# Performance work log

Hardware: AMD Instinct MI355X
Metric: run time of the kernel (lower is better)

The kernel has to match this reference:

```python
import jax, jax.numpy as jnp
import numpy as np

B = 16384      # batch of Monte Carlo paths
N = 100        # time steps
DIM_W = 3
DT = 0.01
SQRT_DT = DT ** 0.5
SIGMA0 = 0.5   # constant diffusion coefficient (concrete sigma = SIGMA0 * ones(B,1,DIM_W))


def _mlp(x, W1, b1, W2, b2, W3, b3):
    h = jax.nn.relu(x @ W1 + b1)
    h = jax.nn.relu(h @ W2 + b2)
    return h @ W3 + b3


def setup_inputs() -> dict:
    key = jax.random.key(0)
    ks = jax.random.split(key, 8)
    s = 0.1  # modest weight scale for numerical sanity
    return {
        'y0': jnp.ones((1,), jnp.float32),
        'Y0': jnp.zeros((1, 1), jnp.float32),
        'zW1': s * jax.random.normal(ks[0], (2, 64), jnp.float32),
        'zb1': jnp.zeros((64,), jnp.float32),
        'zW2': s * jax.random.normal(ks[1], (64, 64), jnp.float32),
        'zb2': jnp.zeros((64,), jnp.float32),
        'zW3': s * jax.random.normal(ks[2], (64, 3), jnp.float32),
        'zb3': jnp.zeros((3,), jnp.float32),
        'qW1': s * jax.random.normal(ks[3], (2, 64), jnp.float32),
        'qb1': jnp.zeros((64,), jnp.float32),
        'qW2': s * jax.random.normal(ks[4], (64, 64), jnp.float32),
        'qb2': jnp.zeros((64,), jnp.float32),
        'qW3': s * jax.random.normal(ks[5], (64, 1), jnp.float32),
        'qb3': jnp.zeros((1,), jnp.float32),
        'dW': jax.random.normal(ks[6], (N, B, DIM_W), jnp.float32),
        'dZ': jax.random.normal(ks[7], (N, B, DIM_W), jnp.float32),
    }


def reference(y0, Y0, zW1, zb1, zW2, zb2, zW3, zb3,
              qW1, qb1, qW2, qb2, qW3, qb3, dW, dZ):
    y = jnp.broadcast_to(y0.reshape(1, 1), (B, 1))          # (B,1) state
    Y = jnp.broadcast_to(Y0, (B, 1))                         # (B,1) value process
    t = jnp.zeros((B, 1), jnp.float32)

    def step(carry, noise):
        y, Y, t, loss_acc = carry
        dWi, dZi = noise
        inp = jnp.concatenate([t, y], axis=1)                # (B,2)
        z = _mlp(inp, zW1, zb1, zW2, zb2, zW3, zb3)          # (B,3)
        q = _mlp(inp, qW1, qb1, qW2, qb2, qW3, qb3)          # (B,1)
        f = 0.5 * q * q                                      # generator (B,1)
        dw = dWi * SQRT_DT
        dz = dZi * SQRT_DT
        # sigma = SIGMA0 * ones(B,1,DIM_W); bmm(sigma, dw) = SIGMA0 * sum_j dw_j
        diffusion = SIGMA0 * jnp.sum(dw, axis=1, keepdims=True)
        y_new = y + q * DT + diffusion                       # mu = q
        Y_next = Y - f * DT + jnp.sum(z * dw, axis=1, keepdims=True)
        residual = Y_next - (Y - f * DT + jnp.sum(z * dz, axis=1, keepdims=True))
        loss_acc = loss_acc + jnp.mean(residual * residual)
        return (y_new, Y_next, t + DT, loss_acc), None

    (y, Y, t, total_residual_loss), _ = jax.lax.scan(
        step, (y, Y, t, jnp.float32(0.0)), (dW, dZ))
    terminal = y * y                                         # terminal_cost(y)
    terminal_loss = jnp.mean((Y - terminal) ** 2)
    return terminal_loss + total_residual_loss
```

## Files before the change

### kernel.cpp

```cpp
#include <hip/hip_runtime.h>
#include <hip/hip_bf16.h>

#define BATCH   16384
#define NSTEPS  100
#define DT_     0.01f
#define SQRTDT  0.1f
#define SIGMA0_ 0.5f

typedef _Float16  f16x2  __attribute__((ext_vector_type(2)));
typedef _Float16  f16x4  __attribute__((ext_vector_type(4)));
typedef _Float16  f16x8  __attribute__((ext_vector_type(8)));
typedef __fp16    h16x2  __attribute__((ext_vector_type(2)));
typedef float     f32x4  __attribute__((ext_vector_type(4)));

__global__ void zero_out_kernel(float* out) { if (threadIdx.x == 0) out[0] = 0.0f; }

static __device__ __forceinline__ f16x4 pk4(const f32x4& d) {
    union { h16x2 h[2]; f16x4 v; } c;
    c.h[0] = __builtin_amdgcn_cvt_pkrtz(d[0], d[1]);
    c.h[1] = __builtin_amdgcn_cvt_pkrtz(d[2], d[3]);
    return c.v;
}

struct N3 { float a, b, c; };

__launch_bounds__(256, 2)
__global__ void deepbsde_kernel(
    const float* __restrict__ y0,  const float* __restrict__ Y0,
    const float* __restrict__ zW1, const float* __restrict__ zb1,
    const float* __restrict__ zW2, const float* __restrict__ zb2,
    const float* __restrict__ zW3, const float* __restrict__ zb3,
    const float* __restrict__ qW1, const float* __restrict__ qb1,
    const float* __restrict__ qW2, const float* __restrict__ qb2,
    const float* __restrict__ qW3, const float* __restrict__ qb3,
    const float* __restrict__ dW,  const float* __restrict__ dZ,
    float* __restrict__ out)
{
    __shared__ __align__(16) _Float16 tbl[NSTEPS * 128];
    __shared__ float yring[2][NSTEPS + 1][16];
    __shared__ float ffin[2][16];
    __shared__ int   flags[2][2];

    const int tid  = threadIdx.x;
    const int lane = tid & 63;
    const int w    = tid >> 6;
    const int g    = w >> 1;
    const int flip = (((int)blockIdx.x >> 3) ^ ((int)blockIdx.x >> 8)) & 1;
    const bool isQ = ((w & 1) ^ flip) != 0;
    const int ln15 = lane & 15, q4 = lane >> 4;
    const int gw   = (blockIdx.x << 1) + g;
    const int pbase = gw << 4;

    if (tid < 4) ((int*)flags)[tid] = 0;

    {
        float tt = 0.0f;
        for (int i = 0; i < NSTEPS; ++i) {
            int r = (tid - (i << 6)) & 255;
            if (r < 64) {
                int q4e = r >> 4, mlp_ = (r >> 3) & 1, m = r & 7;
                const float* Wp = mlp_ ? qW1 : zW1;
                const float* bp = mlp_ ? qb1 : zb1;
                int i0 = 2*m, i1 = 2*m + 1;
                int k0 = 32*(i0 >> 3) + 8*q4e + (i0 & 7);
                int k1 = 32*(i1 >> 3) + 8*q4e + (i1 & 7);
                _Float16 th = (_Float16)tt;
                f16x2 A = {(_Float16)Wp[k0], (_Float16)Wp[k1]};
                f16x2 C = {(_Float16)bp[k0], (_Float16)bp[k1]};
                f16x2 tv = {th, th};
                f16x2 v = A*tv + C;
                int idx = (i*4 + q4e)*16 + mlp_*8 + m;
                *(f16x2*)&tbl[idx << 1] = v;
            }
            tt += DT_;
        }
    }

    const float* W1p = isQ ? qW1 : zW1;
    const float* W2p = isQ ? qW2 : zW2;
    const float* b2p = isQ ? qb2 : zb2;

    f16x2 B1[8];
#pragma unroll
    for (int m = 0; m < 8; ++m) {
        int i0 = 2*m, i1 = 2*m + 1;
        int k0 = 32*(i0 >> 3) + 8*q4 + (i0 & 7);
        int k1 = 32*(i1 >> 3) + 8*q4 + (i1 & 7);
        B1[m] = (f16x2){(_Float16)W1p[64 + k0], (_Float16)W1p[64 + k1]};
    }

    f16x8 Af[4][2];
#pragma unroll
    for (int tN = 0; tN < 4; ++tN)
#pragma unroll
        for (int f = 0; f < 2; ++f)
#pragma unroll
            for (int j = 0; j < 8; ++j) {
                int k = 32*f + 8*q4 + j, n = 16*tN + ln15;
                Af[tN][f][j] = (_Float16)W2p[k*64 + n];
            }

    f32x4 b2v[4];
#pragma unroll
    for (int tN = 0; tN < 4; ++tN)
#pragma unroll
        for (int r = 0; r < 4; ++r)
            b2v[tN][r] = b2p[16*tN + 4*q4 + r];

    const int c3 = ln15 & 3;
    f16x8 A3[2];
#pragma unroll
    for (int fl = 0; fl < 2; ++fl)
#pragma unroll
        for (int j = 0; j < 8; ++j) {
            int tN = 2*fl + (j >> 2);
            int n  = 16*tN + 4*q4 + (j & 3);
            float wv = isQ ? ((c3 == 3) ? qW3[n]                 : 0.0f)
                           : ((c3 < 3)  ? SQRTDT * zW3[n*3 + c3] : 0.0f);
            A3[fl][j] = (_Float16)wv;
        }

    const f32x4 C3b = isQ ? (f32x4){0.0f, 0.0f, 0.0f, qb3[0]}
                          : (f32x4){SQRTDT*zb3[0], SQRTDT*zb3[1], SQRTDT*zb3[2], 0.0f};

    const float CSIG = SIGMA0_ * SQRTDT;
    const float NHDT = -0.5f * DT_;
    const float y0v = y0[0], Y0v = Y0[0];

    const f16x2 zero2h = {(_Float16)0.0f, (_Float16)0.0f};
    const f16x4 zero4h = {(_Float16)0.0f, (_Float16)0.0f, (_Float16)0.0f, (_Float16)0.0f};

    if (isQ && q4 == 0) *(volatile float*)&yring[g][0][ln15] = y0v;

    __syncthreads();

    auto loadW = [&](int i, N3& d) {
        int ic = (i < NSTEPS) ? i : NSTEPS - 1;
        const float* p = dW + ((size_t)ic * BATCH + pbase + ln15) * 3;
        d.a = p[0]; d.b = p[1]; d.c = p[2];
    };
    auto loadZ = [&](int i, N3& d) {
        int ic = (i < NSTEPS) ? i : NSTEPS - 1;
        const float* p = dZ + ((size_t)ic * BATCH + pbase + ln15) * 3;
        d.a = p[0]; d.b = p[1]; d.c = p[2];
    };

    if (!isQ) {
        float Ysum = 0.0f, acc = 0.0f;
        float ya, yb, yc, yd;

        auto ybatch = [&](int base) {
            volatile int* qf = &flags[g][0];
            while (*qf < base + 4) { }
            ya = *(volatile float*)&yring[g][base + 0][ln15];
            yb = *(volatile float*)&yring[g][base + 1][ln15];
            yc = *(volatile float*)&yring[g][base + 2][ln15];
            yd = *(volatile float*)&yring[g][base + 3][ln15];
        };

        auto zpair = [&](int iA, float yA, int iB, float yB,
                         const N3& wA, const N3& zA, const N3& wB, const N3& zB) {
            const f16x8* tpA = (const f16x8*)(tbl + (iA*4 + q4)*32);
            const f16x8* tpB = (const f16x8*)(tbl + (iB*4 + q4)*32);
            union U8 { f16x8 v; f16x2 h[4]; };
            U8 TA0; TA0.v = tpA[0]; U8 TA1; TA1.v = tpA[1];
            U8 TB0; TB0.v = tpB[0]; U8 TB1; TB1.v = tpB[1];

            _Float16 yhA = (_Float16)yA, yhB = (_Float16)yB;
            const f16x2 yvA = {yhA, yhA}, yvB = {yhB, yhB};
            union { f16x2 h[4]; f16x8 v; } a0, a1, b0, b1;
#pragma unroll
            for (int m = 0; m < 4; ++m) {
                a0.h[m] = __builtin_elementwise_max((f16x2)(B1[m]*yvA   + TA0.h[m]), zero2h);
                b0.h[m] = __builtin_elementwise_max((f16x2)(B1[m]*yvB   + TB0.h[m]), zero2h);
                a1.h[m] = __builtin_elementwise_max((f16x2)(B1[m+4]*yvA + TA1.h[m]), zero2h);
                b1.h[m] = __builtin_elementwise_max((f16x2)(B1[m+4]*yvB + TB1.h[m]), zero2h);
            }

            union { f16x4 q[4]; f16x8 o[2]; } BA, BB;
#pragma unroll
            for (int tN = 0; tN < 4; ++tN) {
                f32x4 dA = b2v[tN];
                f32x4 dB = b2v[tN];
                dA = __builtin_amdgcn_mfma_f32_16x16x32_f16(Af[tN][0], a0.v, dA, 0, 0, 0);
                dB = __builtin_amdgcn_mfma_f32_16x16x32_f16(Af[tN][0], b0.v, dB, 0, 0, 0);
                dA = __builtin_amdgcn_mfma_f32_16x16x32_f16(Af[tN][1], a1.v, dA, 0, 0, 0);
                dB = __builtin_amdgcn_mfma_f32_16x16x32_f16(Af[tN][1], b1.v, dB, 0, 0, 0);
                BA.q[tN] = __builtin_elementwise_max(pk4(dA), zero4h);
                BB.q[tN] = __builtin_elementwise_max(pk4(dB), zero4h);
            }

            f32x4 PA = C3b, PB = C3b;
            PA = __builtin_amdgcn_mfma_f32_16x16x32_f16(A3[0], BA.o[0], PA, 0, 0, 0);
            PB = __builtin_amdgcn_mfma_f32_16x16x32_f16(A3[0], BB.o[0], PB, 0, 0, 0);
            PA = __builtin_amdgcn_mfma_f32_16x16x32_f16(A3[1], BA.o[1], PA, 0, 0, 0);
            PB = __builtin_amdgcn_mfma_f32_16x16x32_f16(A3[1], BB.o[1], PB, 0, 0, 0);

            float zdwA = fmaf(PA[2], wA.c, fmaf(PA[1], wA.b, PA[0]*wA.a));
            float zdzA = fmaf(PA[2], zA.c, fmaf(PA[1], zA.b, PA[0]*zA.a));
            Ysum += zdwA;
            float rA = zdwA - zdzA;
            acc = fmaf(rA, rA, acc);
            float zdwB = fmaf(PB[2], wB.c, fmaf(PB[1], wB.b, PB[0]*wB.a));
            float zdzB = fmaf(PB[2], zB.c, fmaf(PB[1], zB.b, PB[0]*zB.a));
            Ysum += zdwB;
            float rB = zdwB - zdzB;
            acc = fmaf(rB, rB, acc);
        };

        N3 w0,w1,w2,w3,w4,w5,w6,w7, z0,z1,z2,z3,z4,z5,z6,z7;
        loadW(0,w0); loadZ(0,z0); loadW(1,w1); loadZ(1,z1);
        loadW(2,w2); loadZ(2,z2); loadW(3,w3); loadZ(3,z3);
        loadW(4,w4); loadZ(4,z4); loadW(5,w5); loadZ(5,z5);
        loadW(6,w6); loadZ(6,z6); loadW(7,w7); loadZ(7,z7);

#pragma unroll 1
        for (int k = 0; k < 12; ++k) {
            int i = 8*k;
            ybatch(i);
            zpair(i,     ya, i + 1, yb, w0, z0, w1, z1);
            loadW(i + 8,  w0); loadZ(i + 8,  z0);
            loadW(i + 9,  w1); loadZ(i + 9,  z1);
            zpair(i + 2, yc, i + 3, yd, w2, z2, w3, z3);
            loadW(i + 10, w2); loadZ(i + 10, z2);
            loadW(i + 11, w3); loadZ(i + 11, z3);
            ybatch(i + 4);
            zpair(i + 4, ya, i + 5, yb, w4, z4, w5, z5);
            loadW(i + 12, w4); loadZ(i + 12, z4);
            loadW(i + 13, w5); loadZ(i + 13, z5);
            zpair(i + 6, yc, i + 7, yd, w6, z6, w7, z7);
            loadW(i + 14, w6); loadZ(i + 14, z6);
            loadW(i + 15, w7); loadZ(i + 15, z7);
        }
        ybatch(96);
        zpair(96, ya, 97, yb, w0, z0, w1, z1);
        zpair(98, yc, 99, yd, w2, z2, w3, z3);

        {
            volatile int* qf = &flags[g][0];
            while (*qf < NSTEPS + 1) { }
        }
        float Fq = *(volatile float*)&ffin[g][ln15];
        float yT = *(volatile float*)&yring[g][NSTEPS][ln15];
        float Yvf = Y0v + Fq + Ysum;
        float dterm = Yvf - yT*yT;
        acc = fmaf(dterm, dterm, acc);

        float val = (q4 == 0) ? acc : 0.0f;
#pragma unroll
        for (int off = 1; off < 64; off <<= 1) val += __shfl_xor(val, off);
        if (lane == 0) atomicAdd(out, val * (1.0f / BATCH));
    } else {
        __builtin_amdgcn_s_setprio(1);
        float y = y0v, Facc = 0.0f;
        f16x8 c0, c1, d0, d1;
        { const f16x8* tp = (const f16x8*)(tbl + q4*32); c0 = tp[2]; c1 = tp[3]; }

        auto qbody = [&](int j, const N3& nw, f16x8& t0, f16x8& t1, f16x8& u0, f16x8& u1) {
            int jp = j + 1; jp = (jp > NSTEPS - 1) ? NSTEPS - 1 : jp;
            { const f16x8* tp = (const f16x8*)(tbl + (jp*4 + q4)*32); u0 = tp[2]; u1 = tp[3]; }

            _Float16 yh = (_Float16)y;
            const f16x2 yv = {yh, yh};
            union U8 { f16x8 v; f16x2 h[4]; };
            U8 T0; T0.v = t0; U8 T1; T1.v = t1;
            union { f16x2 h[4]; f16x8 v; } b0, b1;
#pragma unroll
            for (int m = 0; m < 4; ++m) {
                b0.h[m] = __builtin_elementwise_max((f16x2)(B1[m]*yv   + T0.h[m]), zero2h);
                b1.h[m] = __builtin_elementwise_max((f16x2)(B1[m+4]*yv + T1.h[m]), zero2h);
            }
            union { f16x4 q[4]; f16x8 o[2]; } Bh;
#pragma unroll
            for (int tN = 0; tN < 4; ++tN) {
                f32x4 d = b2v[tN];
                d = __builtin_amdgcn_mfma_f32_16x16x32_f16(Af[tN][0], b0.v, d, 0, 0, 0);
                d = __builtin_amdgcn_mfma_f32_16x16x32_f16(Af[tN][1], b1.v, d, 0, 0, 0);
                Bh.q[tN] = __builtin_elementwise_max(pk4(d), zero4h);
            }
            f32x4 Pv = C3b;
            Pv = __builtin_amdgcn_mfma_f32_16x16x32_f16(A3[0], Bh.o[0], Pv, 0, 0, 0);
            Pv = __builtin_amdgcn_mfma_f32_16x16x32_f16(A3[1], Bh.o[1], Pv, 0, 0, 0);

            float qv = Pv[3];
            float snw = (nw.a + nw.b) + nw.c;
            Facc = fmaf(NHDT*qv, qv, Facc);
            y = fmaf(CSIG, snw, fmaf(qv, DT_, y));
            if (q4 == 0) *(volatile float*)&yring[g][j + 1][ln15] = y;
        };

        N3 n0,n1,n2,n3,n4,n5,n6,n7;
        loadW(0,n0); loadW(1,n1); loadW(2,n2); loadW(3,n3);
        loadW(4,n4); loadW(5,n5); loadW(6,n6); loadW(7,n7);

#pragma unroll 1
        for (int k = 0; k < 12; ++k) {
            int j = 8*k;
            qbody(j,     n0, c0, c1, d0, d1);  loadW(j + 8,  n0);
            qbody(j + 1, n1, d0, d1, c0, c1);  loadW(j + 9,  n1);
            qbody(j + 2, n2, c0, c1, d0, d1);  loadW(j + 10, n2);
            qbody(j + 3, n3, d0, d1, c0, c1);  loadW(j + 11, n3);
            __builtin_amdgcn_s_waitcnt(0xC07F);
            if (lane == 0) *(volatile int*)&flags[g][0] = j + 4;
            qbody(j + 4, n4, c0, c1, d0, d1);  loadW(j + 12, n4);
            qbody(j + 5, n5, d0, d1, c0, c1);  loadW(j + 13, n5);
            qbody(j + 6, n6, c0, c1, d0, d1);  loadW(j + 14, n6);
            qbody(j + 7, n7, d0, d1, c0, c1);  loadW(j + 15, n7);
            __builtin_amdgcn_s_waitcnt(0xC07F);
            if (lane == 0) *(volatile int*)&flags[g][0] = j + 8;
        }
        qbody(96, n0, c0, c1, d0, d1);
        qbody(97, n1, d0, d1, c0, c1);
        qbody(98, n2, c0, c1, d0, d1);
        qbody(99, n3, d0, d1, c0, c1);
        __builtin_amdgcn_s_waitcnt(0xC07F);
        if (lane == 0) *(volatile int*)&flags[g][0] = NSTEPS;

        if (q4 == 0) *(volatile float*)&ffin[g][ln15] = Facc;
        __builtin_amdgcn_s_waitcnt(0xC07F);
        if (lane == 0) *(volatile int*)&flags[g][0] = NSTEPS + 1;
    }
}

extern "C" void kernel_launch(void* const* d_in, const int* in_sizes, int n_in,
                              void* d_out, int out_size, void* d_ws, size_t ws_size,
                              hipStream_t stream)
{
    zero_out_kernel<<<1, 64, 0, stream>>>((float*)d_out);
    deepbsde_kernel<<<512, 256, 0, stream>>>(
        (const float*)d_in[0],  (const float*)d_in[1],
        (const float*)d_in[2],  (const float*)d_in[3],
        (const float*)d_in[4],  (const float*)d_in[5],
        (const float*)d_in[6],  (const float*)d_in[7],
        (const float*)d_in[8],  (const float*)d_in[9],
        (const float*)d_in[10], (const float*)d_in[11],
        (const float*)d_in[12], (const float*)d_in[13],
        (const float*)d_in[14], (const float*)d_in[15],
        (float*)d_out);
}
```

Baseline: 159.3 us.

## Split z-MLP across two waves per 16-path group, one q wave producer

Each block now handles a single 16-path group with three waves: one wave runs the serial q-MLP recurrence and two waves each compute half of the z-MLP hidden layer. They exchange partial output-layer sums through an LDS ring guarded by flags. The y values passed to the z waves are stored as fp16 in LDS, and the q wave no longer prefetches its time table one step ahead. The aim is to shorten the per-step z critical path by splitting its MFMA work so the z consumers keep up with the serial q producer, at the cost of more blocks, extra LDS handshakes and an added spin-wait dependency between the two z waves.

After: 195.2 us. +22.5%, slower.

```diff
diff --git a/kernel.cpp b/kernel.cpp
--- a/kernel.cpp
+++ b/kernel.cpp
@@ -23,8 +23,9 @@
 }
 
 struct N3 { float a, b, c; };
-
-__launch_bounds__(256, 2)
+union HU { unsigned short u; _Float16 h; };
+
+__launch_bounds__(192, 3)
 __global__ void deepbsde_kernel(
     const float* __restrict__ y0,  const float* __restrict__ Y0,
     const float* __restrict__ zW1, const float* __restrict__ zb1,
@@ -37,27 +38,26 @@
     float* __restrict__ out)
 {
     __shared__ __align__(16) _Float16 tbl[NSTEPS * 128];
-    __shared__ float yring[2][NSTEPS + 1][16];
-    __shared__ float ffin[2][16];
-    __shared__ int   flags[2][2];
+    __shared__ unsigned short yh_ring[NSTEPS + 1][16];
+    __shared__ float rB_ring[NSTEPS][16];
+    __shared__ float ffin[16], yTfin[16], Bfin[16];
+    __shared__ int   flags[2];
 
     const int tid  = threadIdx.x;
     const int lane = tid & 63;
     const int w    = tid >> 6;
-    const int g    = w >> 1;
-    const int flip = (((int)blockIdx.x >> 3) ^ ((int)blockIdx.x >> 8)) & 1;
-    const bool isQ = ((w & 1) ^ flip) != 0;
     const int ln15 = lane & 15, q4 = lane >> 4;
-    const int gw   = (blockIdx.x << 1) + g;
-    const int pbase = gw << 4;
-
-    if (tid < 4) ((int*)flags)[tid] = 0;
+    const int pbase = (int)blockIdx.x << 4;
+
+    const float y0v = y0[0], Y0v = Y0[0];
+    if (tid < 2) flags[tid] = 0;
+    if (tid < 16) { HU hu; hu.h = (_Float16)y0v; yh_ring[0][tid] = hu.u; }
 
     {
         float tt = 0.0f;
         for (int i = 0; i < NSTEPS; ++i) {
-            int r = (tid - (i << 6)) & 255;
-            if (r < 64) {
+            int r = tid - ((i % 3) << 6);
+            if (r >= 0 && r < 64) {
                 int q4e = r >> 4, mlp_ = (r >> 3) & 1, m = r & 7;
                 const float* Wp = mlp_ ? qW1 : zW1;
                 const float* bp = mlp_ ? qb1 : zb1;
@@ -75,64 +75,11 @@
             tt += DT_;
         }
     }
-
-    const float* W1p = isQ ? qW1 : zW1;
-    const float* W2p = isQ ? qW2 : zW2;
-    const float* b2p = isQ ? qb2 : zb2;
-
-    f16x2 B1[8];
-#pragma unroll
-    for (int m = 0; m < 8; ++m) {
-        int i0 = 2*m, i1 = 2*m + 1;
-        int k0 = 32*(i0 >> 3) + 8*q4 + (i0 & 7);
-        int k1 = 32*(i1 >> 3) + 8*q4 + (i1 & 7);
-        B1[m] = (f16x2){(_Float16)W1p[64 + k0], (_Float16)W1p[64 + k1]};
-    }
-
-    f16x8 Af[4][2];
-#pragma unroll
-    for (int tN = 0; tN < 4; ++tN)
-#pragma unroll
-        for (int f = 0; f < 2; ++f)
-#pragma unroll
-            for (int j = 0; j < 8; ++j) {
-                int k = 32*f + 8*q4 + j, n = 16*tN + ln15;
-                Af[tN][f][j] = (_Float16)W2p[k*64 + n];
-            }
-
-    f32x4 b2v[4];
-#pragma unroll
-    for (int tN = 0; tN < 4; ++tN)
-#pragma unroll
-        for (int r = 0; r < 4; ++r)
-            b2v[tN][r] = b2p[16*tN + 4*q4 + r];
-
-    const int c3 = ln15 & 3;
-    f16x8 A3[2];
-#pragma unroll
-    for (int fl = 0; fl < 2; ++fl)
-#pragma unroll
-        for (int j = 0; j < 8; ++j) {
-            int tN = 2*fl + (j >> 2);
-            int n  = 16*tN + 4*q4 + (j & 3);
-            float wv = isQ ? ((c3 == 3) ? qW3[n]                 : 0.0f)
-                           : ((c3 < 3)  ? SQRTDT * zW3[n*3 + c3] : 0.0f);
-            A3[fl][j] = (_Float16)wv;
-        }
-
-    const f32x4 C3b = isQ ? (f32x4){0.0f, 0.0f, 0.0f, qb3[0]}
-                          : (f32x4){SQRTDT*zb3[0], SQRTDT*zb3[1], SQRTDT*zb3[2], 0.0f};
-
-    const float CSIG = SIGMA0_ * SQRTDT;
-    const float NHDT = -0.5f * DT_;
-    const float y0v = y0[0], Y0v = Y0[0];
+    __syncthreads();
 
     const f16x2 zero2h = {(_Float16)0.0f, (_Float16)0.0f};
     const f16x4 zero4h = {(_Float16)0.0f, (_Float16)0.0f, (_Float16)0.0f, (_Float16)0.0f};
-
-    if (isQ && q4 == 0) *(volatile float*)&yring[g][0][ln15] = y0v;
-
-    __syncthreads();
+    const int c3 = ln15 & 3;
 
     auto loadW = [&](int i, N3& d) {
         int ic = (i < NSTEPS) ? i : NSTEPS - 1;
@@ -145,67 +92,99 @@
         d.a = p[0]; d.b = p[1]; d.c = p[2];
     };
 
-    if (!isQ) {
+    if (w < 2) {
+        const int half = w;
+        f16x2 B1[8];
+#pragma unroll
+        for (int m = 0; m < 8; ++m) {
+            int i0 = 2*m, i1 = 2*m + 1;
+            int k0 = 32*(i0 >> 3) + 8*q4 + (i0 & 7);
+            int k1 = 32*(i1 >> 3) + 8*q4 + (i1 & 7);
+            B1[m] = (f16x2){(_Float16)zW1[64 + k0], (_Float16)zW1[64 + k1]};
+        }
+        f16x8 Af[2][2];
+#pragma unroll
+        for (int tl = 0; tl < 2; ++tl)
+#pragma unroll
+            for (int f = 0; f < 2; ++f)
+#pragma unroll
+                for (int j = 0; j < 8; ++j) {
+                    int tN = 2*half + tl;
+                    int k = 32*f + 8*q4 + j, n = 16*tN + ln15;
+                    Af[tl][f][j] = (_Float16)zW2[k*64 + n];
+                }
+        f32x4 b2v[2];
+#pragma unroll
+        for (int tl = 0; tl < 2; ++tl)
+#pragma unroll
+            for (int r = 0; r < 4; ++r)
+                b2v[tl][r] = zb2[16*(2*half + tl) + 4*q4 + r];
+        f16x8 A3h;
+#pragma unroll
+        for (int j = 0; j < 8; ++j) {
+            int tN = 2*half + (j >> 2);
+            int n  = 16*tN + 4*q4 + (j & 3);
+            A3h[j] = (_Float16)((c3 < 3) ? SQRTDT * zW3[n*3 + c3] : 0.0f);
+        }
+        const f32x4 C3b = (half == 0)
+            ? (f32x4){SQRTDT*zb3[0], SQRTDT*zb3[1], SQRTDT*zb3[2], 0.0f}
+            : (f32x4){0.0f, 0.0f, 0.0f, 0.0f};
+
         float Ysum = 0.0f, acc = 0.0f;
-        float ya, yb, yc, yd;
+        _Float16 ya, yb, yc, yd;
+        float ra = 0.f, rb = 0.f, rc = 0.f, rd = 0.f;
 
         auto ybatch = [&](int base) {
-            volatile int* qf = &flags[g][0];
+            volatile int* qf = &flags[0];
             while (*qf < base + 4) { }
-            ya = *(volatile float*)&yring[g][base + 0][ln15];
-            yb = *(volatile float*)&yring[g][base + 1][ln15];
-            yc = *(volatile float*)&yring[g][base + 2][ln15];
-            yd = *(volatile float*)&yring[g][base + 3][ln15];
+            HU h0, h1_, h2, h3;
+            h0.u = *(volatile unsigned short*)&yh_ring[base + 0][ln15];
+            h1_.u = *(volatile unsigned short*)&yh_ring[base + 1][ln15];
+            h2.u = *(volatile unsigned short*)&yh_ring[base + 2][ln15];
+            h3.u = *(volatile unsigned short*)&yh_ring[base + 3][ln15];
+            ya = h0.h; yb = h1_.h; yc = h2.h; yd = h3.h;
         };
-
-        auto zpair = [&](int iA, float yA, int iB, float yB,
-                         const N3& wA, const N3& zA, const N3& wB, const N3& zB) {
-            const f16x8* tpA = (const f16x8*)(tbl + (iA*4 + q4)*32);
-            const f16x8* tpB = (const f16x8*)(tbl + (iB*4 + q4)*32);
+        auto rbatch = [&](int base) {
+            volatile int* bf = &flags[1];
+            while (*bf < base + 4) { }
+            ra = *(volatile float*)&rB_ring[base + 0][ln15];
+            rb = *(volatile float*)&rB_ring[base + 1][ln15];
+            rc = *(volatile float*)&rB_ring[base + 2][ln15];
+            rd = *(volatile float*)&rB_ring[base + 3][ln15];
+        };
+
+        auto zstep = [&](int i, _Float16 yh, const N3& nw, const N3& nz, float rOther) {
+            const f16x8* tp = (const f16x8*)(tbl + (i*4 + q4)*32);
             union U8 { f16x8 v; f16x2 h[4]; };
-            U8 TA0; TA0.v = tpA[0]; U8 TA1; TA1.v = tpA[1];
-            U8 TB0; TB0.v = tpB[0]; U8 TB1; TB1.v = tpB[1];
-
-            _Float16 yhA = (_Float16)yA, yhB = (_Float16)yB;
-            const f16x2 yvA = {yhA, yhA}, yvB = {yhB, yhB};
-            union { f16x2 h[4]; f16x8 v; } a0, a1, b0, b1;
+            U8 T0; T0.v = tp[0]; U8 T1; T1.v = tp[1];
+            const f16x2 yv = {yh, yh};
+            union { f16x2 h[4]; f16x8 v; } b0, b1;
 #pragma unroll
             for (int m = 0; m < 4; ++m) {
-                a0.h[m] = __builtin_elementwise_max((f16x2)(B1[m]*yvA   + TA0.h[m]), zero2h);
-                b0.h[m] = __builtin_elementwise_max((f16x2)(B1[m]*yvB   + TB0.h[m]), zero2h);
-                a1.h[m] = __builtin_elementwise_max((f16x2)(B1[m+4]*yvA + TA1.h[m]), zero2h);
-                b1.h[m] = __builtin_elementwise_max((f16x2)(B1[m+4]*yvB + TB1.h[m]), zero2h);
-            }
-
-            union { f16x4 q[4]; f16x8 o[2]; } BA, BB;
-#pragma unroll
-            for (int tN = 0; tN < 4; ++tN) {
-                f32x4 dA = b2v[tN];
-                f32x4 dB = b2v[tN];
-                dA = __builtin_amdgcn_mfma_f32_16x16x32_f16(Af[tN][0], a0.v, dA, 0, 0, 0);
-                dB = __builtin_amdgcn_mfma_f32_16x16x32_f16(Af[tN][0], b0.v, dB, 0, 0, 0);
-                dA = __builtin_amdgcn_mfma_f32_16x16x32_f16(Af[tN][1], a1.v, dA, 0, 0, 0);
-                dB = __builtin_amdgcn_mfma_f32_16x16x32_f16(Af[tN][1], b1.v, dB, 0, 0, 0);
-                BA.q[tN] = __builtin_elementwise_max(pk4(dA), zero4h);
-                BB.q[tN] = __builtin_elementwise_max(pk4(dB), zero4h);
-            }
-
-            f32x4 PA = C3b, PB = C3b;
-            PA = __builtin_amdgcn_mfma_f32_16x16x32_f16(A3[0], BA.o[0], PA, 0, 0, 0);
-            PB = __builtin_amdgcn_mfma_f32_16x16x32_f16(A3[0], BB.o[0], PB, 0, 0, 0);
-            PA = __builtin_amdgcn_mfma_f32_16x16x32_f16(A3[1], BA.o[1], PA, 0, 0, 0);
-            PB = __builtin_amdgcn_mfma_f32_16x16x32_f16(A3[1], BB.o[1], PB, 0, 0, 0);
-
-            float zdwA = fmaf(PA[2], wA.c, fmaf(PA[1], wA.b, PA[0]*wA.a));
-            float zdzA = fmaf(PA[2], zA.c, fmaf(PA[1], zA.b, PA[0]*zA.a));
-            Ysum += zdwA;
-            float rA = zdwA - zdzA;
-            acc = fmaf(rA, rA, acc);
-            float zdwB = fmaf(PB[2], wB.c, fmaf(PB[1], wB.b, PB[0]*wB.a));
-            float zdzB = fmaf(PB[2], zB.c, fmaf(PB[1], zB.b, PB[0]*zB.a));
-            Ysum += zdwB;
-            float rB = zdwB - zdzB;
-            acc = fmaf(rB, rB, acc);
+                b0.h[m] = __builtin_elementwise_max((f16x2)(B1[m]*yv   + T0.h[m]), zero2h);
+                b1.h[m] = __builtin_elementwise_max((f16x2)(B1[m+4]*yv + T1.h[m]), zero2h);
+            }
+            f32x4 d0 = b2v[0];
+            d0 = __builtin_amdgcn_mfma_f32_16x16x32_f16(Af[0][0], b0.v, d0, 0, 0, 0);
+            d0 = __builtin_amdgcn_mfma_f32_16x16x32_f16(Af[0][1], b1.v, d0, 0, 0, 0);
+            f32x4 d1 = b2v[1];
+            d1 = __builtin_amdgcn_mfma_f32_16x16x32_f16(Af[1][0], b0.v, d1, 0, 0, 0);
+            d1 = __builtin_amdgcn_mfma_f32_16x16x32_f16(Af[1][1], b1.v, d1, 0, 0, 0);
+            union { f16x4 q[2]; f16x8 o; } B3;
+            B3.q[0] = __builtin_elementwise_max(pk4(d0), zero4h);
+            B3.q[1] = __builtin_elementwise_max(pk4(d1), zero4h);
+            f32x4 P = C3b;
+            P = __builtin_amdgcn_mfma_f32_16x16x32_f16(A3h, B3.o, P, 0, 0, 0);
+            float zdw = fmaf(P[2], nw.c, fmaf(P[1], nw.b, P[0]*nw.a));
+            float zdz = fmaf(P[2], nz.c, fmaf(P[1], nz.b, P[0]*nz.a));
+            Ysum += zdw;
+            float rh = zdw - zdz;
+            if (half == 0) {
+                float r = rh + rOther;
+                acc = fmaf(r, r, acc);
+            } else {
+                if (q4 == 0) *(volatile float*)&rB_ring[i][ln15] = rh;
+            }
         };
 
         N3 w0,w1,w2,w3,w4,w5,w6,w7, z0,z1,z2,z3,z4,z5,z6,z7;
@@ -218,52 +197,101 @@
         for (int k = 0; k < 12; ++k) {
             int i = 8*k;
             ybatch(i);
-            zpair(i,     ya, i + 1, yb, w0, z0, w1, z1);
-            loadW(i + 8,  w0); loadZ(i + 8,  z0);
-            loadW(i + 9,  w1); loadZ(i + 9,  z1);
-            zpair(i + 2, yc, i + 3, yd, w2, z2, w3, z3);
-            loadW(i + 10, w2); loadZ(i + 10, z2);
-            loadW(i + 11, w3); loadZ(i + 11, z3);
+            if (half == 0) rbatch(i);
+            zstep(i,     ya, w0, z0, ra); loadW(i + 8,  w0); loadZ(i + 8,  z0);
+            zstep(i + 1, yb, w1, z1, rb); loadW(i + 9,  w1); loadZ(i + 9,  z1);
+            zstep(i + 2, yc, w2, z2, rc); loadW(i + 10, w2); loadZ(i + 10, z2);
+            zstep(i + 3, yd, w3, z3, rd); loadW(i + 11, w3); loadZ(i + 11, z3);
+            if (half == 1) {
+                __builtin_amdgcn_s_waitcnt(0xC07F);
+                if (lane == 0) *(volatile int*)&flags[1] = i + 4;
+            }
             ybatch(i + 4);
-            zpair(i + 4, ya, i + 5, yb, w4, z4, w5, z5);
-            loadW(i + 12, w4); loadZ(i + 12, z4);
-            loadW(i + 13, w5); loadZ(i + 13, z5);
-            zpair(i + 6, yc, i + 7, yd, w6, z6, w7, z7);
-            loadW(i + 14, w6); loadZ(i + 14, z6);
-            loadW(i + 15, w7); loadZ(i + 15, z7);
+            if (half == 0) rbatch(i + 4);
+            zstep(i + 4, ya, w4, z4, ra); loadW(i + 12, w4); loadZ(i + 12, z4);
+            zstep(i + 5, yb, w5, z5, rb); loadW(i + 13, w5); loadZ(i + 13, z5);
+            zstep(i + 6, yc, w6, z6, rc); loadW(i + 14, w6); loadZ(i + 14, z6);
+            zstep(i + 7, yd, w7, z7, rd); loadW(i + 15, w7); loadZ(i + 15, z7);
+            if (half == 1) {
+                __builtin_amdgcn_s_waitcnt(0xC07F);
+                if (lane == 0) *(volatile int*)&flags[1] = i + 8;
+            }
         }
         ybatch(96);
-        zpair(96, ya, 97, yb, w0, z0, w1, z1);
-        zpair(98, yc, 99, yd, w2, z2, w3, z3);
-
-        {
-            volatile int* qf = &flags[g][0];
-            while (*qf < NSTEPS + 1) { }
-        }
-        float Fq = *(volatile float*)&ffin[g][ln15];
-        float yT = *(volatile float*)&yring[g][NSTEPS][ln15];
-        float Yvf = Y0v + Fq + Ysum;
-        float dterm = Yvf - yT*yT;
-        acc = fmaf(dterm, dterm, acc);
-
-        float val = (q4 == 0) ? acc : 0.0f;
-#pragma unroll
-        for (int off = 1; off < 64; off <<= 1) val += __shfl_xor(val, off);
-        if (lane == 0) atomicAdd(out, val * (1.0f / BATCH));
+        if (half == 0) rbatch(96);
+        zstep(96, ya, w0, z0, ra);
+        zstep(97, yb, w1, z1, rb);
+        zstep(98, yc, w2, z2, rc);
+        zstep(99, yd, w3, z3, rd);
+
+        if (half == 1) {
+            __builtin_amdgcn_s_waitcnt(0xC07F);
+            if (lane == 0) *(volatile int*)&flags[1] = NSTEPS;
+            if (q4 == 0) *(volatile float*)&Bfin[ln15] = Ysum;
+            __builtin_amdgcn_s_waitcnt(0xC07F);
+            if (lane == 0) *(volatile int*)&flags[1] = NSTEPS + 1;
+        } else {
+            { volatile int* qf = &flags[0]; while (*qf < NSTEPS + 1) { } }
+            { volatile int* bf = &flags[1]; while (*bf < NSTEPS + 1) { } }
+            float Fq    = *(volatile float*)&ffin[ln15];
+            float YsumB = *(volatile float*)&Bfin[ln15];
+            float yT    = *(volatile float*)&yTfin[ln15];
+            float Yvf = Y0v + Fq + (Ysum + YsumB);
+            float dterm = Yvf - yT*yT;
+            acc = fmaf(dterm, dterm, acc);
+
+            float val = (q4 == 0) ? acc : 0.0f;
+#pragma unroll
+            for (int off = 1; off < 64; off <<= 1) val += __shfl_xor(val, off);
+            if (lane == 0) atomicAdd(out, val * (1.0f / BATCH));
+        }
     } else {
         __builtin_amdgcn_s_setprio(1);
+        f16x2 B1[8];
+#pragma unroll
+        for (int m = 0; m < 8; ++m) {
+            int i0 = 2*m, i1 = 2*m + 1;
+            int k0 = 32*(i0 >> 3) + 8*q4 + (i0 & 7);
+            int k1 = 32*(i1 >> 3) + 8*q4 + (i1 & 7);
+            B1[m] = (f16x2){(_Float16)qW1[64 + k0], (_Float16)qW1[64 + k1]};
+        }
+        f16x8 Af[4][2];
+#pragma unroll
+        for (int tN = 0; tN < 4; ++tN)
+#pragma unroll
+            for (int f = 0; f < 2; ++f)
+#pragma unroll
+                for (int j = 0; j < 8; ++j) {
+                    int k = 32*f + 8*q4 + j, n = 16*tN + ln15;
+                    Af[tN][f][j] = (_Float16)qW2[k*64 + n];
+                }
+        f32x4 b2v[4];
+#pragma unroll
+        for (int tN = 0; tN < 4; ++tN)
+#pragma unroll
+            for (int r = 0; r < 4; ++r)
+                b2v[tN][r] = qb2[16*tN + 4*q4 + r];
+        f16x8 A3q[2];
+#pragma unroll
+        for (int fl = 0; fl < 2; ++fl)
+#pragma unroll
+            for (int j = 0; j < 8; ++j) {
+                int tN = 2*fl + (j >> 2);
+                int n  = 16*tN + 4*q4 + (j & 3);
+                A3q[fl][j] = (_Float16)((c3 == 3) ? qW3[n] : 0.0f);
+            }
+        const f32x4 C3bq = {0.0f, 0.0f, 0.0f, qb3[0]};
+        const float CSIG = SIGMA0_ * SQRTDT;
+        const float NHDT = -0.5f * DT_;
+
         float y = y0v, Facc = 0.0f;
-        f16x8 c0, c1, d0, d1;
-        { const f16x8* tp = (const f16x8*)(tbl + q4*32); c0 = tp[2]; c1 = tp[3]; }
-
-        auto qbody = [&](int j, const N3& nw, f16x8& t0, f16x8& t1, f16x8& u0, f16x8& u1) {
-            int jp = j + 1; jp = (jp > NSTEPS - 1) ? NSTEPS - 1 : jp;
-            { const f16x8* tp = (const f16x8*)(tbl + (jp*4 + q4)*32); u0 = tp[2]; u1 = tp[3]; }
-
+
+        auto qstep = [&](int j, const N3& nw) {
+            const f16x8* tp = (const f16x8*)(tbl + (j*4 + q4)*32);
+            union U8 { f16x8 v; f16x2 h[4]; };
+            U8 T0; T0.v = tp[2]; U8 T1; T1.v = tp[3];
             _Float16 yh = (_Float16)y;
             const f16x2 yv = {yh, yh};
-            union U8 { f16x8 v; f16x2 h[4]; };
-            U8 T0; T0.v = t0; U8 T1; T1.v = t1;
             union { f16x2 h[4]; f16x8 v; } b0, b1;
 #pragma unroll
             for (int m = 0; m < 4; ++m) {
@@ -278,15 +306,18 @@
                 d = __builtin_amdgcn_mfma_f32_16x16x32_f16(Af[tN][1], b1.v, d, 0, 0, 0);
                 Bh.q[tN] = __builtin_elementwise_max(pk4(d), zero4h);
             }
-            f32x4 Pv = C3b;
-            Pv = __builtin_amdgcn_mfma_f32_16x16x32_f16(A3[0], Bh.o[0], Pv, 0, 0, 0);
-            Pv = __builtin_amdgcn_mfma_f32_16x16x32_f16(A3[1], Bh.o[1], Pv, 0, 0, 0);
+            f32x4 Pv = C3bq;
+            Pv = __builtin_amdgcn_mfma_f32_16x16x32_f16(A3q[0], Bh.o[0], Pv, 0, 0, 0);
+            Pv = __builtin_amdgcn_mfma_f32_16x16x32_f16(A3q[1], Bh.o[1], Pv, 0, 0, 0);
 
             float qv = Pv[3];
             float snw = (nw.a + nw.b) + nw.c;
             Facc = fmaf(NHDT*qv, qv, Facc);
             y = fmaf(CSIG, snw, fmaf(qv, DT_, y));
-            if (q4 == 0) *(volatile float*)&yring[g][j + 1][ln15] = y;
+            if (q4 == 0) {
+                HU hu; hu.h = (_Float16)y;
+                *(volatile unsigned short*)&yh_ring[j + 1][ln15] = hu.u;
+            }
         };
 
         N3 n0,n1,n2,n3,n4,n5,n6,n7;
@@ -296,29 +327,32 @@
 #pragma unroll 1
         for (int k = 0; k < 12; ++k) {
             int j = 8*k;
-            qbody(j,     n0, c0, c1, d0, d1);  loadW(j + 8,  n0);
-            qbody(j + 1, n1, d0, d1, c0, c1);  loadW(j + 9,  n1);
-            qbody(j + 2, n2, c0, c1, d0, d1);  loadW(j + 10, n2);
-            qbody(j + 3, n3, d0, d1, c0, c1);  loadW(j + 11, n3);
+            qstep(j,     n0);  loadW(j + 8,  n0);
+            qstep(j + 1, n1);  loadW(j + 9,  n1);
+            qstep(j + 2, n2);  loadW(j + 10, n2);
+            qstep(j + 3, n3);  loadW(j + 11, n3);
             __builtin_amdgcn_s_waitcnt(0xC07F);
-            if (lane == 0) *(volatile int*)&flags[g][0] = j + 4;
-            qbody(j + 4, n4, c0, c1, d0, d1);  loadW(j + 12, n4);
-            qbody(j + 5, n5, d0, d1, c0, c1);  loadW(j + 13, n5);
-            qbody(j + 6, n6, c0, c1, d0, d1);  loadW(j + 14, n6);
-            qbody(j + 7, n7, d0, d1, c0, c1);  loadW(j + 15, n7);
+            if (lane == 0) *(volatile int*)&flags[0] = j + 4;
+            qstep(j + 4, n4);  loadW(j + 12, n4);
+            qstep(j + 5, n5);  loadW(j + 13, n5);
+            qstep(j + 6, n6);  loadW(j + 14, n6);
+            qstep(j + 7, n7);  loadW(j + 15, n7);
             __builtin_amdgcn_s_waitcnt(0xC07F);
-            if (lane == 0) *(volatile int*)&flags[g][0] = j + 8;
-        }
-        qbody(96, n0, c0, c1, d0, d1);
-        qbody(97, n1, d0, d1, c0, c1);
-        qbody(98, n2, c0, c1, d0, d1);
-        qbody(99, n3, d0, d1, c0, c1);
+            if (lane == 0) *(volatile int*)&flags[0] = j + 8;
+        }
+        qstep(96, n0);
+        qstep(97, n1);
+        qstep(98, n2);
+        qstep(99, n3);
         __builtin_amdgcn_s_waitcnt(0xC07F);
-        if (lane == 0) *(volatile int*)&flags[g][0] = NSTEPS;
-
-        if (q4 == 0) *(volatile float*)&ffin[g][ln15] = Facc;
+        if (lane == 0) *(volatile int*)&flags[0] = NSTEPS;
+
+        if (q4 == 0) {
+            *(volatile float*)&ffin[ln15]  = Facc;
+            *(volatile float*)&yTfin[ln15] = y;
+        }
         __builtin_amdgcn_s_waitcnt(0xC07F);
-        if (lane == 0) *(volatile int*)&flags[g][0] = NSTEPS + 1;
+        if (lane == 0) *(volatile int*)&flags[0] = NSTEPS + 1;
     }
 }
 
@@ -327,7 +361,7 @@
                               hipStream_t stream)
 {
     zero_out_kernel<<<1, 64, 0, stream>>>((float*)d_out);
-    deepbsde_kernel<<<512, 256, 0, stream>>>(
+    deepbsde_kernel<<<1024, 192, 0, stream>>>(
         (const float*)d_in[0],  (const float*)d_in[1],
         (const float*)d_in[2],  (const float*)d_in[3],
         (const float*)d_in[4],  (const float*)d_in[5],
```

## Restructure z-wave consumer into single-step pipeline with fp16 y ring and prefetch

Applied to the files above, without the earlier changes.

The z-MLP wave now processes one step at a time instead of interleaving two independent steps. Each step prefetches the next step's time-table entries from LDS. The y values it waits on are polled one batch ahead, so the spin-wait overlaps with compute. The y ring passed from the q-wave is stored as fp16 bits and converted once by the producer, and the terminal y goes in a separate fp32 slot. This cuts the wait latency and conversion work on the consumer's critical path, but gives up the two-way MFMA interleave that hid MFMA latency.

Result: no change. 161.3 us (+1.2%).

```diff
diff --git a/kernel.cpp b/kernel.cpp
--- a/kernel.cpp
+++ b/kernel.cpp
@@ -23,6 +23,7 @@
 }
 
 struct N3 { float a, b, c; };
+union HU { unsigned short u; _Float16 h; };
 
 __launch_bounds__(256, 2)
 __global__ void deepbsde_kernel(
@@ -37,9 +38,9 @@
     float* __restrict__ out)
 {
     __shared__ __align__(16) _Float16 tbl[NSTEPS * 128];
-    __shared__ float yring[2][NSTEPS + 1][16];
-    __shared__ float ffin[2][16];
-    __shared__ int   flags[2][2];
+    __shared__ unsigned short yh_ring[2][NSTEPS + 1][16];
+    __shared__ float ffin[2][16], yTfin[2][16];
+    __shared__ int   flags[2];
 
     const int tid  = threadIdx.x;
     const int lane = tid & 63;
@@ -51,7 +52,9 @@
     const int gw   = (blockIdx.x << 1) + g;
     const int pbase = gw << 4;
 
-    if (tid < 4) ((int*)flags)[tid] = 0;
+    const float y0v = y0[0], Y0v = Y0[0];
+    if (tid < 2) flags[tid] = 0;
+    if (tid < 32) { HU hu; hu.h = (_Float16)y0v; yh_ring[tid >> 4][0][tid & 15] = hu.u; }
 
     {
         float tt = 0.0f;
@@ -88,7 +91,6 @@
         int k1 = 32*(i1 >> 3) + 8*q4 + (i1 & 7);
         B1[m] = (f16x2){(_Float16)W1p[64 + k0], (_Float16)W1p[64 + k1]};
     }
-
     f16x8 Af[4][2];
 #pragma unroll
     for (int tN = 0; tN < 4; ++tN)
@@ -99,7 +101,6 @@
                 int k = 32*f + 8*q4 + j, n = 16*tN + ln15;
                 Af[tN][f][j] = (_Float16)W2p[k*64 + n];
             }
-
     f32x4 b2v[4];
 #pragma unroll
     for (int tN = 0; tN < 4; ++tN)
@@ -119,20 +120,13 @@
                            : ((c3 < 3)  ? SQRTDT * zW3[n*3 + c3] : 0.0f);
             A3[fl][j] = (_Float16)wv;
         }
-
     const f32x4 C3b = isQ ? (f32x4){0.0f, 0.0f, 0.0f, qb3[0]}
                           : (f32x4){SQRTDT*zb3[0], SQRTDT*zb3[1], SQRTDT*zb3[2], 0.0f};
 
     const float CSIG = SIGMA0_ * SQRTDT;
     const float NHDT = -0.5f * DT_;
-    const float y0v = y0[0], Y0v = Y0[0];
-
     const f16x2 zero2h = {(_Float16)0.0f, (_Float16)0.0f};
     const f16x4 zero4h = {(_Float16)0.0f, (_Float16)0.0f, (_Float16)0.0f, (_Float16)0.0f};
-
-    if (isQ && q4 == 0) *(volatile float*)&yring[g][0][ln15] = y0v;
-
-    __syncthreads();
 
     auto loadW = [&](int i, N3& d) {
         int ic = (i < NSTEPS) ? i : NSTEPS - 1;
@@ -145,69 +139,56 @@
         d.a = p[0]; d.b = p[1]; d.c = p[2];
     };
 
+    __syncthreads();
+
     if (!isQ) {
         float Ysum = 0.0f, acc = 0.0f;
-        float ya, yb, yc, yd;
-
-        auto ybatch = [&](int base) {
-            volatile int* qf = &flags[g][0];
-            while (*qf < base + 4) { }
-            ya = *(volatile float*)&yring[g][base + 0][ln15];
-            yb = *(volatile float*)&yring[g][base + 1][ln15];
-            yc = *(volatile float*)&yring[g][base + 2][ln15];
-            yd = *(volatile float*)&yring[g][base + 3][ln15];
+        f16x8 tc0, tc1, td0, td1;
+        { const f16x8* tp = (const f16x8*)(tbl + q4*32); tc0 = tp[0]; tc1 = tp[1]; }
+        unsigned short ya, yb, yc, yd, ea, eb, ec, ed;
+
+        auto zstep = [&](int i, unsigned short yu, const N3& nw, const N3& nz,
+                         f16x8& t0, f16x8& t1, f16x8& u0, f16x8& u1) {
+            int ip = i + 1; ip = (ip > NSTEPS - 1) ? NSTEPS - 1 : ip;
+            { const f16x8* tp = (const f16x8*)(tbl + (ip*4 + q4)*32); u0 = tp[0]; u1 = tp[1]; }
+
+            HU hu; hu.u = yu;
+            const f16x2 yv = {hu.h, hu.h};
+            union U8 { f16x8 v; f16x2 h[4]; };
+            U8 T0; T0.v = t0; U8 T1; T1.v = t1;
+            union { f16x2 h[4]; f16x8 v; } b0, b1;
+#pragma unroll
+            for (int m = 0; m < 4; ++m) {
+                b0.h[m] = __builtin_elementwise_max((f16x2)(B1[m]*yv   + T0.h[m]), zero2h);
+                b1.h[m] = __builtin_elementwise_max((f16x2)(B1[m+4]*yv + T1.h[m]), zero2h);
+            }
+            union { f16x4 q[4]; f16x8 o[2]; } Bh;
+#pragma unroll
+            for (int tN = 0; tN < 4; ++tN) {
+                f32x4 d = b2v[tN];
+                d = __builtin_amdgcn_mfma_f32_16x16x32_f16(Af[tN][0], b0.v, d, 0, 0, 0);
+                d = __builtin_amdgcn_mfma_f32_16x16x32_f16(Af[tN][1], b1.v, d, 0, 0, 0);
+                Bh.q[tN] = __builtin_elementwise_max(pk4(d), zero4h);
+            }
+            f32x4 P = C3b;
+            P = __builtin_amdgcn_mfma_f32_16x16x32_f16(A3[0], Bh.o[0], P, 0, 0, 0);
+            P = __builtin_amdgcn_mfma_f32_16x16x32_f16(A3[1], Bh.o[1], P, 0, 0, 0);
+
+            float zdw = fmaf(P[2], nw.c, fmaf(P[1], nw.b, P[0]*nw.a));
+            float zdz = fmaf(P[2], nz.c, fmaf(P[1], nz.b, P[0]*nz.a));
+            Ysum += zdw;
+            float r = zdw - zdz;
+            acc = fmaf(r, r, acc);
         };
 
-        auto zpair = [&](int iA, float yA, int iB, float yB,
-                         const N3& wA, const N3& zA, const N3& wB, const N3& zB) {
-            const f16x8* tpA = (const f16x8*)(tbl + (iA*4 + q4)*32);
-            const f16x8* tpB = (const f16x8*)(tbl + (iB*4 + q4)*32);
-            union U8 { f16x8 v; f16x2 h[4]; };
-            U8 TA0; TA0.v = tpA[0]; U8 TA1; TA1.v = tpA[1];
-            U8 TB0; TB0.v = tpB[0]; U8 TB1; TB1.v = tpB[1];
-
-            _Float16 yhA = (_Float16)yA, yhB = (_Float16)yB;
-            const f16x2 yvA = {yhA, yhA}, yvB = {yhB, yhB};
-            union { f16x2 h[4]; f16x8 v; } a0, a1, b0, b1;
-#pragma unroll
-            for (int m = 0; m < 4; ++m) {
-                a0.h[m] = __builtin_elementwise_max((f16x2)(B1[m]*yvA   + TA0.h[m]), zero2h);
-                b0.h[m] = __builtin_elementwise_max((f16x2)(B1[m]*yvB   + TB0.h[m]), zero2h);
-                a1.h[m] = __builtin_elementwise_max((f16x2)(B1[m+4]*yvA + TA1.h[m]), zero2h);
-                b1.h[m] = __builtin_elementwise_max((f16x2)(B1[m+4]*yvB + TB1.h[m]), zero2h);
-            }
-
-            union { f16x4 q[4]; f16x8 o[2]; } BA, BB;
-#pragma unroll
-            for (int tN = 0; tN < 4; ++tN) {
-                f32x4 dA = b2v[tN];
-                f32x4 dB = b2v[tN];
-                dA = __builtin_amdgcn_mfma_f32_16x16x32_f16(Af[tN][0], a0.v, dA, 0, 0, 0);
-                dB = __builtin_amdgcn_mfma_f32_16x16x32_f16(Af[tN][0], b0.v, dB, 0, 0, 0);
-                dA = __builtin_amdgcn_mfma_f32_16x16x32_f16(Af[tN][1], a1.v, dA, 0, 0, 0);
-                dB = __builtin_amdgcn_mfma_f32_16x16x32_f16(Af[tN][1], b1.v, dB, 0, 0, 0);
-                BA.q[tN] = __builtin_elementwise_max(pk4(dA), zero4h);
-                BB.q[tN] = __builtin_elementwise_max(pk4(dB), zero4h);
-            }
-
-            f32x4 PA = C3b, PB = C3b;
-            PA = __builtin_amdgcn_mfma_f32_16x16x32_f16(A3[0], BA.o[0], PA, 0, 0, 0);
-            PB = __builtin_amdgcn_mfma_f32_16x16x32_f16(A3[0], BB.o[0], PB, 0, 0, 0);
-            PA = __builtin_amdgcn_mfma_f32_16x16x32_f16(A3[1], BA.o[1], PA, 0, 0, 0);
-            PB = __builtin_amdgcn_mfma_f32_16x16x32_f16(A3[1], BB.o[1], PB, 0, 0, 0);
-
-            float zdwA = fmaf(PA[2], wA.c, fmaf(PA[1], wA.b, PA[0]*wA.a));
-            float zdzA = fmaf(PA[2], zA.c, fmaf(PA[1], zA.b, PA[0]*zA.a));
-            Ysum += zdwA;
-            float rA = zdwA - zdzA;
-            acc = fmaf(rA, rA, acc);
-            float zdwB = fmaf(PB[2], wB.c, fmaf(PB[1], wB.b, PB[0]*wB.a));
-            float zdzB = fmaf(PB[2], zB.c, fmaf(PB[1], zB.b, PB[0]*zB.a));
-            Ysum += zdwB;
-            float rB = zdwB - zdzB;
-            acc = fmaf(rB, rB, acc);
-        };
-
+        {
+            volatile int* qf = &flags[g];
+            while (*qf < 4) { }
+            ya = *(volatile unsigned short*)&yh_ring[g][0][ln15];
+            yb = *(volatile unsigned short*)&yh_ring[g][1][ln15];
+            yc = *(volatile unsigned short*)&yh_ring[g][2][ln15];
+            yd = *(volatile unsigned short*)&yh_ring[g][3][ln15];
+        }
         N3 w0,w1,w2,w3,w4,w5,w6,w7, z0,z1,z2,z3,z4,z5,z6,z7;
         loadW(0,w0); loadZ(0,z0); loadW(1,w1); loadZ(1,z1);
         loadW(2,w2); loadZ(2,z2); loadW(3,w3); loadZ(3,z3);
@@ -215,33 +196,34 @@
         loadW(6,w6); loadZ(6,z6); loadW(7,w7); loadZ(7,z7);
 
 #pragma unroll 1
-        for (int k = 0; k < 12; ++k) {
-            int i = 8*k;
-            ybatch(i);
-            zpair(i,     ya, i + 1, yb, w0, z0, w1, z1);
-            loadW(i + 8,  w0); loadZ(i + 8,  z0);
-            loadW(i + 9,  w1); loadZ(i + 9,  z1);
-            zpair(i + 2, yc, i + 3, yd, w2, z2, w3, z3);
-            loadW(i + 10, w2); loadZ(i + 10, z2);
-            loadW(i + 11, w3); loadZ(i + 11, z3);
-            ybatch(i + 4);
-            zpair(i + 4, ya, i + 5, yb, w4, z4, w5, z5);
-            loadW(i + 12, w4); loadZ(i + 12, z4);
-            loadW(i + 13, w5); loadZ(i + 13, z5);
-            zpair(i + 6, yc, i + 7, yd, w6, z6, w7, z7);
-            loadW(i + 14, w6); loadZ(i + 14, z6);
-            loadW(i + 15, w7); loadZ(i + 15, z7);
-        }
-        ybatch(96);
-        zpair(96, ya, 97, yb, w0, z0, w1, z1);
-        zpair(98, yc, 99, yd, w2, z2, w3, z3);
-
-        {
-            volatile int* qf = &flags[g][0];
-            while (*qf < NSTEPS + 1) { }
-        }
+        for (int b = 0; b < 25; ++b) {
+            int i = 4*b;
+            if (b < 24) {
+                int need = i + 8; if (need > NSTEPS) need = NSTEPS;
+                volatile int* qf = &flags[g];
+                while (*qf < need) { }
+                ea = *(volatile unsigned short*)&yh_ring[g][i + 4][ln15];
+                eb = *(volatile unsigned short*)&yh_ring[g][i + 5][ln15];
+                ec = *(volatile unsigned short*)&yh_ring[g][i + 6][ln15];
+                ed = *(volatile unsigned short*)&yh_ring[g][i + 7][ln15];
+            }
+            if ((b & 1) == 0) {
+                zstep(i,     ya, w0, z0, tc0, tc1, td0, td1); loadW(i + 8,  w0); loadZ(i + 8,  z0);
+                zstep(i + 1, yb, w1, z1, td0, td1, tc0, tc1); loadW(i + 9,  w1); loadZ(i + 9,  z1);
+                zstep(i + 2, yc, w2, z2, tc0, tc1, td0, td1); loadW(i + 10, w2); loadZ(i + 10, z2);
+                zstep(i + 3, yd, w3, z3, td0, td1, tc0, tc1); loadW(i + 11, w3); loadZ(i + 11, z3);
+            } else {
+                zstep(i,     ya, w4, z4, tc0, tc1, td0, td1); loadW(i + 8,  w4); loadZ(i + 8,  z4);
+                zstep(i + 1, yb, w5, z5, td0, td1, tc0, tc1); loadW(i + 9,  w5); loadZ(i + 9,  z5);
+                zstep(i + 2, yc, w6, z6, tc0, tc1, td0, td1); loadW(i + 10, w6); loadZ(i + 10, z6);
+                zstep(i + 3, yd, w7, z7, td0, td1, tc0, tc1); loadW(i + 11, w7); loadZ(i + 11, z7);
+            }
+            ya = ea; yb = eb; yc = ec; yd = ed;
+        }
+
+        { volatile int* qf = &flags[g]; while (*qf < NSTEPS + 1) { } }
         float Fq = *(volatile float*)&ffin[g][ln15];
-        float yT = *(volatile float*)&yring[g][NSTEPS][ln15];
+        float yT = *(volatile float*)&yTfin[g][ln15];
         float Yvf = Y0v + Fq + Ysum;
         float dterm = Yvf - yT*yT;
         acc = fmaf(dterm, dterm, acc);
@@ -256,7 +238,7 @@
         f16x8 c0, c1, d0, d1;
         { const f16x8* tp = (const f16x8*)(tbl + q4*32); c0 = tp[2]; c1 = tp[3]; }
 
-        auto qbody = [&](int j, const N3& nw, f16x8& t0, f16x8& t1, f16x8& u0, f16x8& u1) {
+        auto qstep = [&](int j, const N3& nw, f16x8& t0, f16x8& t1, f16x8& u0, f16x8& u1) {
             int jp = j + 1; jp = (jp > NSTEPS - 1) ? NSTEPS - 1 : jp;
             { const f16x8* tp = (const f16x8*)(tbl + (jp*4 + q4)*32); u0 = tp[2]; u1 = tp[3]; }
 
@@ -286,7 +268,10 @@
             float snw = (nw.a + nw.b) + nw.c;
             Facc = fmaf(NHDT*qv, qv, Facc);
             y = fmaf(CSIG, snw, fmaf(qv, DT_, y));
-            if (q4 == 0) *(volatile float*)&yring[g][j + 1][ln15] = y;
+            if (q4 == 0) {
+                HU hu; hu.h = (_Float16)y;
+                *(volatile unsigned short*)&yh_ring[g][j + 1][ln15] = hu.u;
+            }
         };
 
         N3 n0,n1,n2,n3,n4,n5,n6,n7;
@@ -296,29 +281,32 @@
 #pragma unroll 1
         for (int k = 0; k < 12; ++k) {
             int j = 8*k;
-            qbody(j,     n0, c0, c1, d0, d1);  loadW(j + 8,  n0);
-            qbody(j + 1, n1, d0, d1, c0, c1);  loadW(j + 9,  n1);
-            qbody(j + 2, n2, c0, c1, d0, d1);  loadW(j + 10, n2);
-            qbody(j + 3, n3, d0, d1, c0, c1);  loadW(j + 11, n3);
+            qstep(j,     n0, c0, c1, d0, d1);  loadW(j + 8,  n0);
+            qstep(j + 1, n1, d0, d1, c0, c1);  loadW(j + 9,  n1);
+            qstep(j + 2, n2, c0, c1, d0, d1);  loadW(j + 10, n2);
+            qstep(j + 3, n3, d0, d1, c0, c1);  loadW(j + 11, n3);
             __builtin_amdgcn_s_waitcnt(0xC07F);
-            if (lane == 0) *(volatile int*)&flags[g][0] = j + 4;
-            qbody(j + 4, n4, c0, c1, d0, d1);  loadW(j + 12, n4);
-            qbody(j + 5, n5, d0, d1, c0, c1);  loadW(j + 13, n5);
-            qbody(j + 6, n6, c0, c1, d0, d1);  loadW(j + 14, n6);
-            qbody(j + 7, n7, d0, d1, c0, c1);  loadW(j + 15, n7);
+            if (lane == 0) *(volatile int*)&flags[g] = j + 4;
+            qstep(j + 4, n4, c0, c1, d0, d1);  loadW(j + 12, n4);
+            qstep(j + 5, n5, d0, d1, c0, c1);  loadW(j + 13, n5);
+            qstep(j + 6, n6, c0, c1, d0, d1);  loadW(j + 14, n6);
+            qstep(j + 7, n7, d0, d1, c0, c1);  loadW(j + 15, n7);
             __builtin_amdgcn_s_waitcnt(0xC07F);
-            if (lane == 0) *(volatile int*)&flags[g][0] = j + 8;
-        }
-        qbody(96, n0, c0, c1, d0, d1);
-        qbody(97, n1, d0, d1, c0, c1);
-        qbody(98, n2, c0, c1, d0, d1);
-        qbody(99, n3, d0, d1, c0, c1);
+            if (lane == 0) *(volatile int*)&flags[g] = j + 8;
+        }
+        qstep(96, n0, c0, c1, d0, d1);
+        qstep(97, n1, d0, d1, c0, c1);
+        qstep(98, n2, c0, c1, d0, d1);
+        qstep(99, n3, d0, d1, c0, c1);
         __builtin_amdgcn_s_waitcnt(0xC07F);
-        if (lane == 0) *(volatile int*)&flags[g][0] = NSTEPS;
-
-        if (q4 == 0) *(volatile float*)&ffin[g][ln15] = Facc;
+        if (lane == 0) *(volatile int*)&flags[g] = NSTEPS;
+
+        if (q4 == 0) {
+            *(volatile float*)&ffin[g][ln15]  = Facc;
+            *(volatile float*)&yTfin[g][ln15] = y;
+        }
         __builtin_amdgcn_s_waitcnt(0xC07F);
-        if (lane == 0) *(volatile int*)&flags[g][0] = NSTEPS + 1;
+        if (lane == 0) *(volatile int*)&flags[g] = NSTEPS + 1;
     }
 }
 
```
